# Kernel tuning notes

Hardware: AMD Instinct MI355X
Metric: run time of the kernel (lower is better)

Reference implementation:

```python
import jax, jax.numpy as jnp
import numpy as np

BATCH = 16384
N_FEATURES = 768
FT_OUT = 1024
ACTIVE_P = 32.0 / 768.0  # ~32 active features per board, like real positions


def setup_inputs() -> dict:
    key = jax.random.key(0)
    k1, k2, k3, k4, k5, k6 = jax.random.split(key, 6)
    # densified sparse one-hot boards: binary {0,1} with ~32/768 density
    board_stm = (jax.random.uniform(k1, (BATCH, N_FEATURES)) < ACTIVE_P).astype(jnp.float32)
    board_nstm = (jax.random.uniform(k2, (BATCH, N_FEATURES)) < ACTIVE_P).astype(jnp.float32)
    # Linear(768, FT_OUT): weight [out, in], bias [out]
    W_ft = jax.random.normal(k3, (FT_OUT, N_FEATURES), dtype=jnp.float32) * (1.0 / np.sqrt(N_FEATURES))
    b_ft = jax.random.normal(k4, (FT_OUT,), dtype=jnp.float32) * 0.01
    # Linear(2*FT_OUT, 1)
    W_out = jax.random.normal(k5, (1, 2 * FT_OUT), dtype=jnp.float32) * (1.0 / np.sqrt(2 * FT_OUT))
    b_out = jax.random.normal(k6, (1,), dtype=jnp.float32) * 0.01
    return {"board_stm": board_stm, "board_nstm": board_nstm,
            "W_ft": W_ft, "b_ft": b_ft, "W_out": W_out, "b_out": b_out}


def screlu(x):
    # SCReLU: clamp(x, 0, 1)^2
    return jnp.square(jnp.clip(x, 0.0, 1.0))


def reference(board_stm, board_nstm, W_ft, b_ft, W_out, b_out):
    # feature transformer applied to both perspectives (shared weights)
    stm = jnp.einsum('bf,of->bo', board_stm, W_ft) + b_ft   # [B, FT_OUT]
    nstm = jnp.einsum('bf,of->bo', board_nstm, W_ft) + b_ft  # [B, FT_OUT]
    hidden = screlu(jnp.concatenate([stm, nstm], axis=1))    # [B, 2*FT_OUT]
    out = jnp.einsum('bh,oh->bo', hidden, W_out) + b_out     # [B, 1]
    return jax.nn.sigmoid(out)
```

## Files before the change

kernel.cpp:

```cpp
#include <hip/hip_runtime.h>
#include <stdint.h>

#define BATCH 16384
#define NF 768
#define FT 1024
#define RB 32
#define GR (2 * RB)
#define ALD 784
#define NW 8
#define THREADS 512

typedef int i32x4 __attribute__((ext_vector_type(4)));

__global__ __launch_bounds__(192) void prep_wq(const float* __restrict__ W_ft,
                                               char* __restrict__ Wq,
                                               float* __restrict__ invs) {
    const int o = blockIdx.x;
    const int t = threadIdx.x;
    __shared__ float smax[3];
    __shared__ float sscale;
    const float4 v = *(const float4*)(W_ft + (size_t)o * NF + t * 4);
    float m = fmaxf(fmaxf(fabsf(v.x), fabsf(v.y)), fmaxf(fabsf(v.z), fabsf(v.w)));
    #pragma unroll
    for (int s = 32; s > 0; s >>= 1) m = fmaxf(m, __shfl_down(m, s, 64));
    if ((t & 63) == 0) smax[t >> 6] = m;
    __syncthreads();
    if (t == 0) {
        const float am = fmaxf(fmaxf(smax[0], smax[1]), smax[2]);
        sscale = 127.0f / am;
        invs[o] = am / 127.0f;
    }
    __syncthreads();
    const float s = sscale;
    const float arr[4] = {v.x, v.y, v.z, v.w};
    uint32_t pk = 0;
    #pragma unroll
    for (int j = 0; j < 4; ++j) {
        const int q = (int)rintf(arr[j] * s);
        pk |= ((uint32_t)(unsigned char)(char)q) << (8 * j);
    }
    *(uint32_t*)(Wq + (size_t)o * NF + t * 4) = pk;
}

__global__ __launch_bounds__(THREADS, 2) void nnue_mfma(
    const float* __restrict__ bstm, const float* __restrict__ bnstm,
    const char* __restrict__ Wq, const float* __restrict__ invs,
    const float* __restrict__ b_ft, const float* __restrict__ W_out,
    const float* __restrict__ b_out, float* __restrict__ out)
{
    __shared__ __align__(16) char Albs[GR * ALD];
    __shared__ float red[GR][NW];

    const int t = threadIdx.x;
    const int w = t >> 6;
    const int l = t & 63;
    const int b0 = blockIdx.x * RB;

    #pragma unroll
    for (int it = 0; it < 24; ++it) {
        const int g = it * THREADS + t;
        const int row = g / 192;
        const int c4 = g - row * 192;
        const float* src = (row < RB) ? (bstm + (size_t)(b0 + row) * NF)
                                      : (bnstm + (size_t)(b0 + row - RB) * NF);
        const float4 v = *(const float4*)(src + c4 * 4);
        const uint32_t pk = (uint32_t)(v.x != 0.0f)
                          | ((uint32_t)(v.y != 0.0f) << 8)
                          | ((uint32_t)(v.z != 0.0f) << 16)
                          | ((uint32_t)(v.w != 0.0f) << 24);
        *(uint32_t*)(Albs + row * ALD + c4 * 4) = pk;
    }
    __syncthreads();

    i32x4 acc[4][8] = {};
    const int cl = l & 15;
    const int q = l >> 4;
    const char* bptr = Wq + (size_t)(w * 128 + cl) * NF + q * 16;
    const int aoff = cl * ALD + q * 16;

    #pragma unroll 2
    for (int ks = 0; ks < 12; ++ks) {
        i32x4 bfrag[8];
        #pragma unroll
        for (int c = 0; c < 8; ++c)
            bfrag[c] = *(const i32x4*)(bptr + c * 16 * NF + ks * 64);
        i32x4 afrag[4];
        #pragma unroll
        for (int r = 0; r < 4; ++r)
            afrag[r] = *(const i32x4*)(Albs + aoff + r * 16 * ALD + ks * 64);
        #pragma unroll
        for (int r = 0; r < 4; ++r)
            #pragma unroll
            for (int c = 0; c < 8; ++c)
                acc[r][c] = __builtin_amdgcn_mfma_i32_16x16x64_i8(
                    afrag[r], bfrag[c], acc[r][c], 0, 0, 0);
    }

    float ps[4][4] = {};
    #pragma unroll
    for (int c = 0; c < 8; ++c) {
        const int col = w * 128 + c * 16 + cl;
        const float iv = invs[col];
        const float bf = b_ft[col];
        const float wo0 = W_out[col];
        const float wo1 = W_out[FT + col];
        #pragma unroll
        for (int r = 0; r < 4; ++r) {
            const float wo = (r < 2) ? wo0 : wo1;
            #pragma unroll
            for (int j = 0; j < 4; ++j) {
                float h = fmaf((float)acc[r][c][j], iv, bf);
                h = fminf(fmaxf(h, 0.0f), 1.0f);
                ps[r][j] = fmaf(h * h, wo, ps[r][j]);
            }
        }
    }
    #pragma unroll
    for (int r = 0; r < 4; ++r)
        #pragma unroll
        for (int j = 0; j < 4; ++j) {
            float v = ps[r][j];
            v += __shfl_xor(v, 1, 64);
            v += __shfl_xor(v, 2, 64);
            v += __shfl_xor(v, 4, 64);
            v += __shfl_xor(v, 8, 64);
            if (cl == 0) red[16 * r + 4 * q + j][w] = v;
        }
    __syncthreads();

    if (t < RB) {
        float x = b_out[0];
        #pragma unroll
        for (int w2 = 0; w2 < NW; ++w2)
            x += red[t][w2] + red[RB + t][w2];
        out[b0 + t] = 1.0f / (1.0f + expf(-x));
    }
}

extern "C" void kernel_launch(void* const* d_in, const int* in_sizes, int n_in,
                              void* d_out, int out_size, void* d_ws, size_t ws_size,
                              hipStream_t stream) {
    const float* board_stm  = (const float*)d_in[0];
    const float* board_nstm = (const float*)d_in[1];
    const float* W_ft       = (const float*)d_in[2];
    const float* b_ft       = (const float*)d_in[3];
    const float* W_out      = (const float*)d_in[4];
    const float* b_out      = (const float*)d_in[5];
    float* out = (float*)d_out;

    char* Wq = (char*)d_ws;
    float* invs = (float*)((char*)d_ws + (size_t)FT * NF);

    prep_wq<<<FT, 192, 0, stream>>>(W_ft, Wq, invs);
    nnue_mfma<<<BATCH / RB, THREADS, 0, stream>>>(board_stm, board_nstm, Wq, invs,
                                                  b_ft, W_out, b_out, out);
}
```

Measured before the change: 76.21 us.

## Double-buffer board chunks across K-steps and split columns over 16 warps

The board tile is no longer staged in full before the MMA loop. Each K-step now loads and packs the next 64-feature chunk into a second LDS buffer while MFMAs run on the current one, with a barrier per step. The block grows to 1024 threads and 16 waves, each covering 64 output columns with a smaller accumulator set, which shrinks LDS use and register pressure. The cost is twelve block-wide barriers per block and less weight reuse per wave.

```diff
diff --git a/kernel.cpp b/kernel.cpp
--- a/kernel.cpp
+++ b/kernel.cpp
@@ -6,9 +6,10 @@
 #define FT 1024
 #define RB 32
 #define GR (2 * RB)
-#define ALD 784
-#define NW 8
-#define THREADS 512
+#define THREADS 1024
+#define NW 16
+#define ALD 80
+#define NKS 12
 
 typedef int i32x4 __attribute__((ext_vector_type(4)));
 
@@ -42,13 +43,18 @@
     *(uint32_t*)(Wq + (size_t)o * NF + t * 4) = pk;
 }
 
-__global__ __launch_bounds__(THREADS, 2) void nnue_mfma(
+__device__ __forceinline__ uint32_t pack01(float4 v) {
+    return (uint32_t)(v.x != 0.0f) | ((uint32_t)(v.y != 0.0f) << 8)
+         | ((uint32_t)(v.z != 0.0f) << 16) | ((uint32_t)(v.w != 0.0f) << 24);
+}
+
+__global__ __launch_bounds__(THREADS, 4) void nnue_mfma(
     const float* __restrict__ bstm, const float* __restrict__ bnstm,
     const char* __restrict__ Wq, const float* __restrict__ invs,
     const float* __restrict__ b_ft, const float* __restrict__ W_out,
     const float* __restrict__ b_out, float* __restrict__ out)
 {
-    __shared__ __align__(16) char Albs[GR * ALD];
+    __shared__ __align__(16) char Abuf[2][GR * ALD];
     __shared__ float red[GR][NW];
 
     const int t = threadIdx.x;
@@ -56,50 +62,49 @@
     const int l = t & 63;
     const int b0 = blockIdx.x * RB;
 
-    #pragma unroll
-    for (int it = 0; it < 24; ++it) {
-        const int g = it * THREADS + t;
-        const int row = g / 192;
-        const int c4 = g - row * 192;
-        const float* src = (row < RB) ? (bstm + (size_t)(b0 + row) * NF)
-                                      : (bnstm + (size_t)(b0 + row - RB) * NF);
-        const float4 v = *(const float4*)(src + c4 * 4);
-        const uint32_t pk = (uint32_t)(v.x != 0.0f)
-                          | ((uint32_t)(v.y != 0.0f) << 8)
-                          | ((uint32_t)(v.z != 0.0f) << 16)
-                          | ((uint32_t)(v.w != 0.0f) << 24);
-        *(uint32_t*)(Albs + row * ALD + c4 * 4) = pk;
-    }
+    const int srow = t >> 4;
+    const int sseg = t & 15;
+    const float* sbase = ((srow < RB) ? (bstm + (size_t)(b0 + srow) * NF)
+                                      : (bnstm + (size_t)(b0 + srow - RB) * NF))
+                         + sseg * 4;
+    const int swr = srow * ALD + sseg * 4;
+
+    *(uint32_t*)(&Abuf[0][swr]) = pack01(*(const float4*)sbase);
     __syncthreads();
 
-    i32x4 acc[4][8] = {};
     const int cl = l & 15;
     const int q = l >> 4;
-    const char* bptr = Wq + (size_t)(w * 128 + cl) * NF + q * 16;
+    const char* bptr = Wq + (size_t)(w * 64 + cl) * NF + q * 16;
     const int aoff = cl * ALD + q * 16;
 
+    i32x4 acc[4][4] = {};
     #pragma unroll 2
-    for (int ks = 0; ks < 12; ++ks) {
-        i32x4 bfrag[8];
+    for (int ks = 0; ks < NKS; ++ks) {
+        const int cur = ks & 1;
+        float4 nv;
+        if (ks < NKS - 1) nv = *(const float4*)(sbase + (ks + 1) * 64);
+        i32x4 bfrag[4];
         #pragma unroll
-        for (int c = 0; c < 8; ++c)
-            bfrag[c] = *(const i32x4*)(bptr + c * 16 * NF + ks * 64);
+        for (int c = 0; c < 4; ++c)
+            bfrag[c] = *(const i32x4*)(bptr + (size_t)c * 16 * NF + ks * 64);
         i32x4 afrag[4];
         #pragma unroll
         for (int r = 0; r < 4; ++r)
-            afrag[r] = *(const i32x4*)(Albs + aoff + r * 16 * ALD + ks * 64);
+            afrag[r] = *(const i32x4*)(&Abuf[cur][aoff + r * 16 * ALD]);
         #pragma unroll
         for (int r = 0; r < 4; ++r)
             #pragma unroll
-            for (int c = 0; c < 8; ++c)
+            for (int c = 0; c < 4; ++c)
                 acc[r][c] = __builtin_amdgcn_mfma_i32_16x16x64_i8(
                     afrag[r], bfrag[c], acc[r][c], 0, 0, 0);
+        if (ks < NKS - 1) *(uint32_t*)(&Abuf[cur ^ 1][swr]) = pack01(nv);
+        __syncthreads();
     }
 
     float ps[4][4] = {};
     #pragma unroll
-    for (int c = 0; c < 8; ++c) {
-        const int col = w * 128 + c * 16 + cl;
+    for (int c = 0; c < 4; ++c) {
+        const int col = w * 64 + c * 16 + cl;
         const float iv = invs[col];
         const float bf = b_ft[col];
         const float wo0 = W_out[col];
```

New measurement: 75.00 us. No clear change (-1.6%).
